# Optimization experiments

Hardware: AMD Instinct MI355X
Metric: run time of the kernel (lower is better)

Reference implementation:

```python
import jax, jax.numpy as jnp
import numpy as np

N = 50000
E = 800000
DIMS = [128, 128, 128, 64, 64]  # n_input, hidden[0], hidden[1], hidden[2], n_output


def setup_inputs() -> dict:
    key = jax.random.key(0)
    ks = jax.random.split(key, 16)
    x = jax.random.normal(ks[0], (N, DIMS[0]), dtype=jnp.float32)
    edge_index = jax.random.randint(ks[1], (2, E), 0, N, dtype=jnp.int64)
    inp = {"x": x, "edge_index": edge_index}
    for i in range(4):
        fan_in, fan_out = DIMS[i], DIMS[i + 1]
        scale = 1.0 / jnp.sqrt(jnp.float32(fan_in))
        inp[f"W{i+1}"] = jax.random.normal(ks[2 + 2 * i], (fan_in, fan_out), dtype=jnp.float32) * scale
        inp[f"b{i+1}"] = jnp.zeros((fan_out,), dtype=jnp.float32)
    return inp


def _gcn_norm(edge_index):
    # add self-loops, compute symmetric normalization D^-1/2 (A+I) D^-1/2
    loop = jnp.arange(N, dtype=edge_index.dtype)
    src = jnp.concatenate([edge_index[0], loop])
    dst = jnp.concatenate([edge_index[1], loop])
    ones = jnp.ones(src.shape[0], dtype=jnp.float32)
    deg = jax.ops.segment_sum(ones, dst, num_segments=N)
    dinv = jnp.where(deg > 0, jax.lax.rsqrt(deg), 0.0)
    norm = dinv[src] * dinv[dst]  # [E+N]
    return src, dst, norm


def _gcn_conv(x, W, b, src, dst, norm):
    h = x @ W                                   # [N, out]
    msg = h[src] * norm[:, None]                # gather + scale, [E+N, out]
    agg = jax.ops.segment_sum(msg, dst, num_segments=N)
    return agg + b


def reference(x, edge_index, W1, b1, W2, b2, W3, b3, W4, b4):
    src, dst, norm = _gcn_norm(edge_index)
    h = _gcn_conv(x, W1, b1, src, dst, norm)
    h = jax.nn.selu(h)
    h = _gcn_conv(h, W2, b2, src, dst, norm)
    h = jax.nn.selu(h)
    h = _gcn_conv(h, W3, b3, src, dst, norm)
    h = jax.nn.selu(h)
    h = _gcn_conv(h, W4, b4, src, dst, norm)
    # F.normalize(x): L2 row-normalize with eps=1e-12
    nrm = jnp.sqrt(jnp.sum(h * h, axis=1, keepdims=True))
    return h / jnp.maximum(nrm, 1e-12)
```

## Files before the change

kernel.cpp:

```cpp
#include <hip/hip_runtime.h>
#include <math.h>

#define NN 50000
#define NE 800000
#define NBK ((NN + 255) >> 8)
#define EPB 4096
#define BINA_BLOCKS ((NE + EPB - 1) / EPB)
#define EPT (EPB / 256)

typedef __attribute__((ext_vector_type(8))) __bf16 bf16x8;
typedef __attribute__((ext_vector_type(4))) float f32x4;

__device__ __forceinline__ float selu_f(float x) {
    const float scale = 1.0507009873554805f;
    const float alpha = 1.6732632423543772f;
    return scale * (x > 0.0f ? x : alpha * expm1f(x));
}

__device__ __forceinline__ unsigned rnd_bf16(float f) {
    unsigned u = __float_as_uint(f);
    return (u + 0x7fffu + ((u >> 16) & 1u)) >> 16;
}
__device__ __forceinline__ unsigned pack_pair(float a, float b) {
    return (rnd_bf16(b) << 16) | rnd_bf16(a);
}
__device__ __forceinline__ float lo_f(unsigned u) { return __uint_as_float(u << 16); }
__device__ __forceinline__ float hi_f(unsigned u) { return __uint_as_float(u & 0xffff0000u); }

__global__ void k_hist(const int* __restrict__ dst, int* __restrict__ cnt) {
    int e = blockIdx.x * blockDim.x + threadIdx.x;
    if (e < NE) atomicAdd(&cnt[dst[e]], 1);
}

#define NB1 ((NN + 1023) / 1024)

__global__ void k_scanA(const int* __restrict__ cnt, int* __restrict__ rowptr,
                        int* __restrict__ partials, float* __restrict__ dinv) {
    __shared__ int wsum[4];
    int tid = threadIdx.x;
    int lane = tid & 63, wave = tid >> 6;
    int base = blockIdx.x * 1024 + tid * 4;
    int e0 = 0, e1 = 0, e2 = 0, e3 = 0;
    if (base + 3 < NN) {
        int4 v = *(const int4*)&cnt[base];
        e0 = v.x; e1 = v.y; e2 = v.z; e3 = v.w;
    } else {
        if (base + 0 < NN) e0 = cnt[base + 0];
        if (base + 1 < NN) e1 = cnt[base + 1];
        if (base + 2 < NN) e2 = cnt[base + 2];
        if (base + 3 < NN) e3 = cnt[base + 3];
    }
    if (base + 0 < NN) dinv[base + 0] = rsqrtf((float)(e0 + 1));
    if (base + 1 < NN) dinv[base + 1] = rsqrtf((float)(e1 + 1));
    if (base + 2 < NN) dinv[base + 2] = rsqrtf((float)(e2 + 1));
    if (base + 3 < NN) dinv[base + 3] = rsqrtf((float)(e3 + 1));

    int lsum = e0 + e1 + e2 + e3;
    int s = lsum;
    #pragma unroll
    for (int off = 1; off < 64; off <<= 1) {
        int t = __shfl_up(s, off, 64);
        if (lane >= off) s += t;
    }
    if (lane == 63) wsum[wave] = s;
    __syncthreads();
    int wbase = 0;
    #pragma unroll
    for (int w = 0; w < 4; w++) wbase += (w < wave) ? wsum[w] : 0;
    int excl = wbase + s - lsum;
    if (base + 0 < NN) rowptr[base + 0] = excl;
    if (base + 1 < NN) rowptr[base + 1] = excl + e0;
    if (base + 2 < NN) rowptr[base + 2] = excl + e0 + e1;
    if (base + 3 < NN) rowptr[base + 3] = excl + e0 + e1 + e2;
    if (tid == 0)
        partials[blockIdx.x] = wsum[0] + wsum[1] + wsum[2] + wsum[3];
}

__global__ void k_scanB(int* __restrict__ partials, int* __restrict__ partials2,
                        int* __restrict__ rowptr) {
    int lane = threadIdx.x;
    int v = (lane < NB1) ? partials[lane] : 0;
    int s = v;
    #pragma unroll
    for (int off = 1; off < 64; off <<= 1) {
        int t = __shfl_up(s, off, 64);
        if (lane >= off) s += t;
    }
    if (lane < NB1) partials2[lane] = s - v;
    if (lane == 63) rowptr[NN] = s;
}

__global__ void k_scanC(int* __restrict__ rowptr, const int* __restrict__ partials2,
                        int* __restrict__ bcur) {
    int off = partials2[blockIdx.x];
    int base = blockIdx.x * 1024 + threadIdx.x * 4;
    #pragma unroll
    for (int j = 0; j < 4; j++) {
        int idx = base + j;
        if (idx < NN) {
            int r = rowptr[idx] + off;
            rowptr[idx] = r;
            if ((idx & 255) == 0) bcur[(idx >> 8) * 16] = r;
        }
    }
}

__global__ void __launch_bounds__(256) k_binA(const int* __restrict__ src,
                                              const int* __restrict__ dst,
                                              int* __restrict__ bcur,
                                              int* __restrict__ tmp) {
    __shared__ int hist[NBK];
    __shared__ int gbase[NBK];
    int tid = threadIdx.x;
    for (int i = tid; i < NBK; i += 256) hist[i] = 0;
    __syncthreads();

    const int e0 = blockIdx.x * EPB;
    int rec[EPT];
    int bs[EPT];
    #pragma unroll
    for (int j = 0; j < EPT; j++) {
        int e = e0 + j * 256 + tid;
        if (e < NE) {
            int s = src[e], d = dst[e];
            int b = d >> 8;
            int slot = atomicAdd(&hist[b], 1);
            rec[j] = (s << 8) | (d & 255);
            bs[j] = (b << 16) | slot;
        } else {
            bs[j] = -1;
        }
    }
    __syncthreads();
    for (int i = tid; i < NBK; i += 256)
        gbase[i] = atomicAdd(&bcur[i * 16], hist[i]);
    __syncthreads();
    #pragma unroll
    for (int j = 0; j < EPT; j++) {
        if (bs[j] >= 0) {
            int b = bs[j] >> 16, slot = bs[j] & 0xffff;
            tmp[gbase[b] + slot] = rec[j];
        }
    }
}

__global__ void __launch_bounds__(256) k_binB(const int* __restrict__ tmp,
                                              const int* __restrict__ rowptr,
                                              const float* __restrict__ dinv,
                                              int2* __restrict__ edat) {
    __shared__ int lpos[256];
    __shared__ float ldin[256];
    int b = blockIdx.x, tid = threadIdx.x;
    int n0 = b << 8;
    int n = n0 + tid;
    if (n < NN) { lpos[tid] = rowptr[n]; ldin[tid] = dinv[n]; }
    int base = rowptr[n0];
    int end  = rowptr[(n0 + 256 < NN) ? n0 + 256 : NN];
    __syncthreads();
    for (int i = base + tid; i < end; i += 256) {
        int rc = tmp[i];
        int s = rc >> 8;
        int dl = rc & 255;
        float nm = dinv[s] * ldin[dl];
        int slot = atomicAdd(&lpos[dl], 1);
        edat[slot] = make_int2(s, __float_as_int(nm));
    }
}

__global__ void k_packx(const float* __restrict__ x, unsigned* __restrict__ tabX) {
    long u = (long)blockIdx.x * 256 + threadIdx.x;
    if (u * 4 < (long)NN * 64) {
        const float4* ip = (const float4*)&x[u * 8];
        float4 a = ip[0], b = ip[1];
        uint4 o;
        o.x = pack_pair(a.x, a.y); o.y = pack_pair(a.z, a.w);
        o.z = pack_pair(b.x, b.y); o.w = pack_pair(b.z, b.w);
        *(uint4*)&tabX[u * 4] = o;
    }
}

__global__ void k_packw(const float* __restrict__ W1, const float* __restrict__ W2,
                        const float* __restrict__ W3, const float* __restrict__ W4,
                        unsigned* __restrict__ Wp) {
    int u = blockIdx.x * 256 + threadIdx.x;
    const float* W; int J, K2, off;
    if (u < 8192)       { W = W1; J = 128; K2 = 64; off = 0; }
    else if (u < 16384) { W = W2; J = 128; K2 = 64; off = 8192; }
    else if (u < 20480) { W = W3; J = 64;  K2 = 64; off = 16384; }
    else if (u < 22528) { W = W4; J = 64;  K2 = 32; off = 20480; }
    else return;
    int v = u - off;
    int col = v / K2, kk = v % K2;
    Wp[u] = pack_pair(W[(2 * kk) * J + col], W[(2 * kk + 1) * J + col]);
}

template <int K, int J>
__global__ void __launch_bounds__(256) k_mm4(const unsigned* __restrict__ tabin,
                                             const unsigned* __restrict__ Wp,
                                             unsigned* __restrict__ out) {
    constexpr int K2 = K / 2;
    constexpr int STRIDE = K2 + 4;
    constexpr int CT = J / 16;
    constexpr int KC = K / 32;
    constexpr int J2 = J / 2;

    __shared__ unsigned Wt[J * STRIDE];

    for (int u4 = threadIdx.x; u4 < J * K2 / 4; u4 += 256) {
        int v = u4 * 4;
        int col = v / K2, kk = v % K2;
        *(uint4*)&Wt[col * STRIDE + kk] = *(const uint4*)&Wp[v];
    }
    __syncthreads();

    const int w = threadIdx.x >> 6, l = threadIdx.x & 63;
    const int lr = l & 15, lk = l >> 4;
    const long r0 = (long)blockIdx.x * 128 + w * 32;

    f32x4 acc[CT][2];
    #pragma unroll
    for (int t = 0; t < CT; t++) {
        acc[t][0] = (f32x4)(0.0f);
        acc[t][1] = (f32x4)(0.0f);
    }

    #pragma unroll
    for (int kc = 0; kc < KC; kc++) {
        uint4 a0u = *(const uint4*)&tabin[(r0 + lr) * K2 + kc * 16 + lk * 4];
        uint4 a1u = *(const uint4*)&tabin[(r0 + 16 + lr) * K2 + kc * 16 + lk * 4];
        bf16x8 a0 = __builtin_bit_cast(bf16x8, a0u);
        bf16x8 a1 = __builtin_bit_cast(bf16x8, a1u);
        #pragma unroll
        for (int t = 0; t < CT; t++) {
            uint4 bu = *(const uint4*)&Wt[(t * 16 + lr) * STRIDE + kc * 16 + lk * 4];
            bf16x8 b = __builtin_bit_cast(bf16x8, bu);
            acc[t][0] = __builtin_amdgcn_mfma_f32_16x16x32_bf16(a0, b, acc[t][0], 0, 0, 0);
            acc[t][1] = __builtin_amdgcn_mfma_f32_16x16x32_bf16(a1, b, acc[t][1], 0, 0, 0);
        }
    }

    #pragma unroll
    for (int t = 0; t < CT; t++) {
        #pragma unroll
        for (int s = 0; s < 2; s++) {
            f32x4 d = acc[t][s];
            #pragma unroll
            for (int i = 0; i < 4; i++) {
                float v = d[i];
                float vp = __shfl_xor(v, 1);
                long row = r0 + s * 16 + lk * 4 + i;
                if (!(l & 1) && row < NN)
                    out[row * J2 + t * 8 + (lr >> 1)] = pack_pair(v, vp);
            }
        }
    }
}

template <bool DO_SELU>
__global__ void k_agg128w(const unsigned* __restrict__ tab, const int* __restrict__ rowptr,
                          const int2* __restrict__ edat, const float* __restrict__ dinv,
                          const float* __restrict__ bias, unsigned* __restrict__ outp) {
    int n = (blockIdx.x * blockDim.x + threadIdx.x) >> 6;
    int l = threadIdx.x & 63;
    if (n >= NN) return;
    int g = l >> 4, sub = l & 15;
    int beg = rowptr[n], end = rowptr[n + 1];

    float ax[8] = {0.f, 0.f, 0.f, 0.f, 0.f, 0.f, 0.f, 0.f};
    int e = beg + g;
    for (; e + 4 < end; e += 8) {
        int2 m0 = edat[e], m1 = edat[e + 4];
        uint4 v0 = *(const uint4*)&tab[(size_t)m0.x * 64 + sub * 4];
        uint4 v1 = *(const uint4*)&tab[(size_t)m1.x * 64 + sub * 4];
        float w0 = __int_as_float(m0.y), w1 = __int_as_float(m1.y);
        ax[0] += w0 * lo_f(v0.x); ax[1] += w0 * hi_f(v0.x);
        ax[2] += w0 * lo_f(v0.y); ax[3] += w0 * hi_f(v0.y);
        ax[4] += w0 * lo_f(v0.z); ax[5] += w0 * hi_f(v0.z);
        ax[6] += w0 * lo_f(v0.w); ax[7] += w0 * hi_f(v0.w);
        ax[0] += w1 * lo_f(v1.x); ax[1] += w1 * hi_f(v1.x);
        ax[2] += w1 * lo_f(v1.y); ax[3] += w1 * hi_f(v1.y);
        ax[4] += w1 * lo_f(v1.z); ax[5] += w1 * hi_f(v1.z);
        ax[6] += w1 * lo_f(v1.w); ax[7] += w1 * hi_f(v1.w);
    }
    for (; e < end; e += 4) {
        int2 m = edat[e];
        uint4 v = *(const uint4*)&tab[(size_t)m.x * 64 + sub * 4];
        float w = __int_as_float(m.y);
        ax[0] += w * lo_f(v.x); ax[1] += w * hi_f(v.x);
        ax[2] += w * lo_f(v.y); ax[3] += w * hi_f(v.y);
        ax[4] += w * lo_f(v.z); ax[5] += w * hi_f(v.z);
        ax[6] += w * lo_f(v.w); ax[7] += w * hi_f(v.w);
    }
    #pragma unroll
    for (int d = 0; d < 8; d++) {
        ax[d] += __shfl_xor(ax[d], 16);
        ax[d] += __shfl_xor(ax[d], 32);
    }
    if (g == 0) {
        float dn = dinv[n];
        float self = dn * dn;
        uint4 su = *(const uint4*)&tab[(size_t)n * 64 + sub * 4];
        float4 b0 = *(const float4*)&bias[sub * 8];
        float4 b1 = *(const float4*)&bias[sub * 8 + 4];
        ax[0] += b0.x + self * lo_f(su.x); ax[1] += b0.y + self * hi_f(su.x);
        ax[2] += b0.z + self * lo_f(su.y); ax[3] += b0.w + self * hi_f(su.y);
        ax[4] += b1.x + self * lo_f(su.z); ax[5] += b1.y + self * hi_f(su.z);
        ax[6] += b1.z + self * lo_f(su.w); ax[7] += b1.w + self * hi_f(su.w);
        if constexpr (DO_SELU) {
            #pragma unroll
            for (int d = 0; d < 8; d++) ax[d] = selu_f(ax[d]);
        }
        uint4 o;
        o.x = pack_pair(ax[0], ax[1]); o.y = pack_pair(ax[2], ax[3]);
        o.z = pack_pair(ax[4], ax[5]); o.w = pack_pair(ax[6], ax[7]);
        *(uint4*)&outp[(size_t)n * 64 + sub * 4] = o;
    }
}

template <bool DO_SELU, bool DO_NORM, bool PACK>
__global__ void k_agg64w(const unsigned* __restrict__ tab, const int* __restrict__ rowptr,
                         const int2* __restrict__ edat, const float* __restrict__ dinv,
                         const float* __restrict__ bias, void* __restrict__ out_) {
    int n = (blockIdx.x * blockDim.x + threadIdx.x) >> 6;
    int l = threadIdx.x & 63;
    if (n >= NN) return;
    int g = l >> 3, sub = l & 7;
    int beg = rowptr[n], end = rowptr[n + 1];

    float ax[8] = {0.f, 0.f, 0.f, 0.f, 0.f, 0.f, 0.f, 0.f};
    int e = beg + g;
    for (; e + 8 < end; e += 16) {
        int2 m0 = edat[e], m1 = edat[e + 8];
        uint4 v0 = *(const uint4*)&tab[(size_t)m0.x * 32 + sub * 4];
        uint4 v1 = *(const uint4*)&tab[(size_t)m1.x * 32 + sub * 4];
        float w0 = __int_as_float(m0.y), w1 = __int_as_float(m1.y);
        ax[0] += w0 * lo_f(v0.x); ax[1] += w0 * hi_f(v0.x);
        ax[2] += w0 * lo_f(v0.y); ax[3] += w0 * hi_f(v0.y);
        ax[4] += w0 * lo_f(v0.z); ax[5] += w0 * hi_f(v0.z);
        ax[6] += w0 * lo_f(v0.w); ax[7] += w0 * hi_f(v0.w);
        ax[0] += w1 * lo_f(v1.x); ax[1] += w1 * hi_f(v1.x);
        ax[2] += w1 * lo_f(v1.y); ax[3] += w1 * hi_f(v1.y);
        ax[4] += w1 * lo_f(v1.z); ax[5] += w1 * hi_f(v1.z);
        ax[6] += w1 * lo_f(v1.w); ax[7] += w1 * hi_f(v1.w);
    }
    for (; e < end; e += 8) {
        int2 m = edat[e];
        uint4 v = *(const uint4*)&tab[(size_t)m.x * 32 + sub * 4];
        float w = __int_as_float(m.y);
        ax[0] += w * lo_f(v.x); ax[1] += w * hi_f(v.x);
        ax[2] += w * lo_f(v.y); ax[3] += w * hi_f(v.y);
        ax[4] += w * lo_f(v.z); ax[5] += w * hi_f(v.z);
        ax[6] += w * lo_f(v.w); ax[7] += w * hi_f(v.w);
    }
    #pragma unroll
    for (int d = 0; d < 8; d++) {
        ax[d] += __shfl_xor(ax[d], 8);
        ax[d] += __shfl_xor(ax[d], 16);
        ax[d] += __shfl_xor(ax[d], 32);
    }
    if (g == 0) {
        float dn = dinv[n];
        float self = dn * dn;
        uint4 su = *(const uint4*)&tab[(size_t)n * 32 + sub * 4];
        float4 b0 = *(const float4*)&bias[sub * 8];
        float4 b1 = *(const float4*)&bias[sub * 8 + 4];
        ax[0] += b0.x + self * lo_f(su.x); ax[1] += b0.y + self * hi_f(su.x);
        ax[2] += b0.z + self * lo_f(su.y); ax[3] += b0.w + self * hi_f(su.y);
        ax[4] += b1.x + self * lo_f(su.z); ax[5] += b1.y + self * hi_f(su.z);
        ax[6] += b1.z + self * lo_f(su.w); ax[7] += b1.w + self * hi_f(su.w);
        if constexpr (DO_SELU) {
            #pragma unroll
            for (int d = 0; d < 8; d++) ax[d] = selu_f(ax[d]);
        }
        if constexpr (DO_NORM) {
            float ss = 0.f;
            #pragma unroll
            for (int d = 0; d < 8; d++) ss += ax[d] * ax[d];
            ss += __shfl_xor(ss, 1);
            ss += __shfl_xor(ss, 2);
            ss += __shfl_xor(ss, 4);
            float inv = 1.0f / fmaxf(sqrtf(ss), 1e-12f);
            #pragma unroll
            for (int d = 0; d < 8; d++) ax[d] *= inv;
        }
        if constexpr (PACK) {
            uint4 o;
            o.x = pack_pair(ax[0], ax[1]); o.y = pack_pair(ax[2], ax[3]);
            o.z = pack_pair(ax[4], ax[5]); o.w = pack_pair(ax[6], ax[7]);
            *(uint4*)&((unsigned*)out_)[(size_t)n * 32 + sub * 4] = o;
        } else {
            float* op = (float*)out_ + (size_t)n * 64 + sub * 8;
            *(float4*)op = make_float4(ax[0], ax[1], ax[2], ax[3]);
            *(float4*)(op + 4) = make_float4(ax[4], ax[5], ax[6], ax[7]);
        }
    }
}

extern "C" void kernel_launch(void* const* d_in, const int* in_sizes, int n_in,
                              void* d_out, int out_size, void* d_ws, size_t ws_size,
                              hipStream_t stream) {
    const float* x  = (const float*)d_in[0];
    const int* edge = (const int*)d_in[1];
    const float* W1 = (const float*)d_in[2]; const float* b1 = (const float*)d_in[3];
    const float* W2 = (const float*)d_in[4]; const float* b2 = (const float*)d_in[5];
    const float* W3 = (const float*)d_in[6]; const float* b3 = (const float*)d_in[7];
    const float* W4 = (const float*)d_in[8]; const float* b4 = (const float*)d_in[9];
    float* out = (float*)d_out;

    char* ws = (char*)d_ws;
    size_t off = 0;
    auto alloc = [&](size_t bytes) -> void* {
        void* p = ws + off;
        off = (off + bytes + 255) & ~(size_t)255;
        return p;
    };
    int*      cnt    = (int*)alloc((size_t)NN * 4);
    int*      rowptr = (int*)alloc((size_t)(NN + 1) * 4);
    float*    dinv   = (float*)alloc((size_t)NN * 4);
    int*      tmp    = (int*)alloc((size_t)NE * 4);
    int2*     edat   = (int2*)alloc((size_t)NE * 8);
    unsigned* tabX   = (unsigned*)alloc((size_t)(NN + 128) * 64 * 4);
    unsigned* tab    = (unsigned*)alloc((size_t)(NN + 128) * 64 * 4);
    unsigned* bufU   = (unsigned*)alloc((size_t)(NN + 128) * 64 * 4);
    unsigned* Wp     = (unsigned*)alloc((size_t)22528 * 4);
    int*      part1  = (int*)alloc(64 * 4);
    int*      part2  = (int*)alloc(64 * 4);
    int*      bcur   = (int*)alloc((size_t)NBK * 16 * 4);

    const int* srcp = edge;
    const int* dstp = edge + NE;

    const int BE = (NE + 255) / 256;

    hipMemsetAsync(cnt, 0, (size_t)NN * 4, stream);
    k_hist<<<BE, 256, 0, stream>>>(dstp, cnt);
    k_scanA<<<NB1, 256, 0, stream>>>(cnt, rowptr, part1, dinv);
    k_scanB<<<1, 64, 0, stream>>>(part1, part2, rowptr);
    k_scanC<<<NB1, 256, 0, stream>>>(rowptr, part2, bcur);
    k_binA<<<BINA_BLOCKS, 256, 0, stream>>>(srcp, dstp, bcur, tmp);
    k_binB<<<NBK, 256, 0, stream>>>(tmp, rowptr, dinv, edat);

    const int AGG_B = (NN + 3) / 4;
    const int MMB = (NN + 127) / 128;
    const int PXB = ((NN * 64 / 4) + 255) / 256;

    k_packw<<<88, 256, 0, stream>>>(W1, W2, W3, W4, Wp);
    k_packx<<<PXB, 256, 0, stream>>>(x, tabX);

    k_mm4<128, 128><<<MMB, 256, 0, stream>>>(tabX, Wp, tab);
    k_agg128w<true><<<AGG_B, 256, 0, stream>>>(tab, rowptr, edat, dinv, b1, bufU);
    k_mm4<128, 128><<<MMB, 256, 0, stream>>>(bufU, Wp + 8192, tab);
    k_agg128w<true><<<AGG_B, 256, 0, stream>>>(tab, rowptr, edat, dinv, b2, bufU);
    k_mm4<128, 64><<<MMB, 256, 0, stream>>>(bufU, Wp + 16384, tab);
    k_agg64w<true, false, true><<<AGG_B, 256, 0, stream>>>(tab, rowptr, edat, dinv, b3, bufU);
    k_mm4<64, 64><<<MMB, 256, 0, stream>>>(bufU, Wp + 20480, tab);
    k_agg64w<false, true, false><<<AGG_B, 256, 0, stream>>>(tab, rowptr, edat, dinv, b4, out);
}
```

Measured before the change: 336.8 us.

## Fold source-side normalization into GEMM epilogue and build CSR with bucket-level scan

Pre-scales each GEMM output row by dinv[row], so aggregation sums plain neighbor rows and applies dinv[dst] once at the end. This lets the per-edge record shrink from an (index, weight) pair to a column index only, halving edge metadata traffic and removing a multiply per edge. The CSR build replaces the per-node histogram and three-stage scan with a bucket histogram and a single-block scan; per-node counts, rowptr and dinv are computed inside the second binning pass. The x-to-bf16 packing kernel is fused into the first GEMM's load path. Rounding changes slightly because the scale is applied before the bf16 conversion.

```diff
diff --git a/kernel.cpp b/kernel.cpp
--- a/kernel.cpp
+++ b/kernel.cpp
@@ -27,36 +27,29 @@
 __device__ __forceinline__ float lo_f(unsigned u) { return __uint_as_float(u << 16); }
 __device__ __forceinline__ float hi_f(unsigned u) { return __uint_as_float(u & 0xffff0000u); }
 
-__global__ void k_hist(const int* __restrict__ dst, int* __restrict__ cnt) {
-    int e = blockIdx.x * blockDim.x + threadIdx.x;
-    if (e < NE) atomicAdd(&cnt[dst[e]], 1);
-}
-
-#define NB1 ((NN + 1023) / 1024)
-
-__global__ void k_scanA(const int* __restrict__ cnt, int* __restrict__ rowptr,
-                        int* __restrict__ partials, float* __restrict__ dinv) {
+__global__ void __launch_bounds__(256) k_histB(const int* __restrict__ dst,
+                                               int* __restrict__ bhist) {
+    __shared__ int h[NBK];
+    for (int i = threadIdx.x; i < NBK; i += 256) h[i] = 0;
+    __syncthreads();
+    int e0 = blockIdx.x * EPB;
+    #pragma unroll
+    for (int j = 0; j < EPT; j++) {
+        int e = e0 + j * 256 + threadIdx.x;
+        if (e < NE) atomicAdd(&h[dst[e] >> 8], 1);
+    }
+    __syncthreads();
+    for (int i = threadIdx.x; i < NBK; i += 256)
+        if (h[i]) atomicAdd(&bhist[i], h[i]);
+}
+
+__global__ void k_scanBkt(const int* __restrict__ bhist, int* __restrict__ bbase,
+                          int* __restrict__ bcur, int* __restrict__ rowptr) {
     __shared__ int wsum[4];
     int tid = threadIdx.x;
     int lane = tid & 63, wave = tid >> 6;
-    int base = blockIdx.x * 1024 + tid * 4;
-    int e0 = 0, e1 = 0, e2 = 0, e3 = 0;
-    if (base + 3 < NN) {
-        int4 v = *(const int4*)&cnt[base];
-        e0 = v.x; e1 = v.y; e2 = v.z; e3 = v.w;
-    } else {
-        if (base + 0 < NN) e0 = cnt[base + 0];
-        if (base + 1 < NN) e1 = cnt[base + 1];
-        if (base + 2 < NN) e2 = cnt[base + 2];
-        if (base + 3 < NN) e3 = cnt[base + 3];
-    }
-    if (base + 0 < NN) dinv[base + 0] = rsqrtf((float)(e0 + 1));
-    if (base + 1 < NN) dinv[base + 1] = rsqrtf((float)(e1 + 1));
-    if (base + 2 < NN) dinv[base + 2] = rsqrtf((float)(e2 + 1));
-    if (base + 3 < NN) dinv[base + 3] = rsqrtf((float)(e3 + 1));
-
-    int lsum = e0 + e1 + e2 + e3;
-    int s = lsum;
+    int v = (tid < NBK) ? bhist[tid] : 0;
+    int s = v;
     #pragma unroll
     for (int off = 1; off < 64; off <<= 1) {
         int t = __shfl_up(s, off, 64);
@@ -67,42 +60,9 @@
     int wbase = 0;
     #pragma unroll
     for (int w = 0; w < 4; w++) wbase += (w < wave) ? wsum[w] : 0;
-    int excl = wbase + s - lsum;
-    if (base + 0 < NN) rowptr[base + 0] = excl;
-    if (base + 1 < NN) rowptr[base + 1] = excl + e0;
-    if (base + 2 < NN) rowptr[base + 2] = excl + e0 + e1;
-    if (base + 3 < NN) rowptr[base + 3] = excl + e0 + e1 + e2;
-    if (tid == 0)
-        partials[blockIdx.x] = wsum[0] + wsum[1] + wsum[2] + wsum[3];
-}
-
-__global__ void k_scanB(int* __restrict__ partials, int* __restrict__ partials2,
-                        int* __restrict__ rowptr) {
-    int lane = threadIdx.x;
-    int v = (lane < NB1) ? partials[lane] : 0;
-    int s = v;
-    #pragma unroll
-    for (int off = 1; off < 64; off <<= 1) {
-        int t = __shfl_up(s, off, 64);
-        if (lane >= off) s += t;
-    }
-    if (lane < NB1) partials2[lane] = s - v;
-    if (lane == 63) rowptr[NN] = s;
-}
-
-__global__ void k_scanC(int* __restrict__ rowptr, const int* __restrict__ partials2,
-                        int* __restrict__ bcur) {
-    int off = partials2[blockIdx.x];
-    int base = blockIdx.x * 1024 + threadIdx.x * 4;
-    #pragma unroll
-    for (int j = 0; j < 4; j++) {
-        int idx = base + j;
-        if (idx < NN) {
-            int r = rowptr[idx] + off;
-            rowptr[idx] = r;
-            if ((idx & 255) == 0) bcur[(idx >> 8) * 16] = r;
-        }
-    }
+    int excl = wbase + s - v;
+    if (tid < NBK) { bbase[tid] = excl; bcur[tid * 16] = excl; }
+    if (tid == 0) { bbase[NBK] = NE; rowptr[NN] = NE; }
 }
 
 __global__ void __launch_bounds__(256) k_binA(const int* __restrict__ src,
@@ -144,38 +104,47 @@
     }
 }
 
-__global__ void __launch_bounds__(256) k_binB(const int* __restrict__ tmp,
-                                              const int* __restrict__ rowptr,
-                                              const float* __restrict__ dinv,
-                                              int2* __restrict__ edat) {
+__global__ void __launch_bounds__(256) k_cntB(const int* __restrict__ tmp,
+                                              const int* __restrict__ bbase,
+                                              int* __restrict__ rowptr,
+                                              float* __restrict__ dinv,
+                                              int* __restrict__ ecol) {
+    __shared__ int cnt256[256];
     __shared__ int lpos[256];
-    __shared__ float ldin[256];
+    __shared__ int wsum[4];
     int b = blockIdx.x, tid = threadIdx.x;
     int n0 = b << 8;
+    cnt256[tid] = 0;
+    __syncthreads();
+    int base = bbase[b], end = bbase[b + 1];
+    for (int i = base + tid; i < end; i += 256)
+        atomicAdd(&cnt256[tmp[i] & 255], 1);
+    __syncthreads();
+    int c = cnt256[tid];
+    int lane = tid & 63, wave = tid >> 6;
+    int s = c;
+    #pragma unroll
+    for (int off = 1; off < 64; off <<= 1) {
+        int t = __shfl_up(s, off, 64);
+        if (lane >= off) s += t;
+    }
+    if (lane == 63) wsum[wave] = s;
+    __syncthreads();
+    int wbase = 0;
+    #pragma unroll
+    for (int w = 0; w < 4; w++) wbase += (w < wave) ? wsum[w] : 0;
+    int excl = base + wbase + s - c;
     int n = n0 + tid;
-    if (n < NN) { lpos[tid] = rowptr[n]; ldin[tid] = dinv[n]; }
-    int base = rowptr[n0];
-    int end  = rowptr[(n0 + 256 < NN) ? n0 + 256 : NN];
+    if (n < NN) {
+        rowptr[n] = excl;
+        dinv[n] = rsqrtf((float)(c + 1));
+    }
+    lpos[tid] = excl;
     __syncthreads();
     for (int i = base + tid; i < end; i += 256) {
         int rc = tmp[i];
-        int s = rc >> 8;
-        int dl = rc & 255;
-        float nm = dinv[s] * ldin[dl];
-        int slot = atomicAdd(&lpos[dl], 1);
-        edat[slot] = make_int2(s, __float_as_int(nm));
-    }
-}
-
-__global__ void k_packx(const float* __restrict__ x, unsigned* __restrict__ tabX) {
-    long u = (long)blockIdx.x * 256 + threadIdx.x;
-    if (u * 4 < (long)NN * 64) {
-        const float4* ip = (const float4*)&x[u * 8];
-        float4 a = ip[0], b = ip[1];
-        uint4 o;
-        o.x = pack_pair(a.x, a.y); o.y = pack_pair(a.z, a.w);
-        o.z = pack_pair(b.x, b.y); o.w = pack_pair(b.z, b.w);
-        *(uint4*)&tabX[u * 4] = o;
+        int slot = atomicAdd(&lpos[rc & 255], 1);
+        ecol[slot] = rc >> 8;
     }
 }
 
@@ -194,9 +163,10 @@
     Wp[u] = pack_pair(W[(2 * kk) * J + col], W[(2 * kk + 1) * J + col]);
 }
 
-template <int K, int J>
-__global__ void __launch_bounds__(256) k_mm4(const unsigned* __restrict__ tabin,
+template <int K, int J, bool INF32>
+__global__ void __launch_bounds__(256) k_mm4(const void* __restrict__ in_,
                                              const unsigned* __restrict__ Wp,
+                                             const float* __restrict__ dinv,
                                              unsigned* __restrict__ out) {
     constexpr int K2 = K / 2;
     constexpr int STRIDE = K2 + 4;
@@ -226,8 +196,24 @@
 
     #pragma unroll
     for (int kc = 0; kc < KC; kc++) {
-        uint4 a0u = *(const uint4*)&tabin[(r0 + lr) * K2 + kc * 16 + lk * 4];
-        uint4 a1u = *(const uint4*)&tabin[(r0 + 16 + lr) * K2 + kc * 16 + lk * 4];
+        uint4 a0u, a1u;
+        if constexpr (INF32) {
+            const float* xin = (const float*)in_;
+            long ra0 = r0 + lr;      if (ra0 >= NN) ra0 = NN - 1;
+            long ra1 = r0 + 16 + lr; if (ra1 >= NN) ra1 = NN - 1;
+            const float4* p0 = (const float4*)&xin[ra0 * K + kc * 32 + lk * 8];
+            const float4* p1 = (const float4*)&xin[ra1 * K + kc * 32 + lk * 8];
+            float4 fa = p0[0], fb = p0[1];
+            a0u.x = pack_pair(fa.x, fa.y); a0u.y = pack_pair(fa.z, fa.w);
+            a0u.z = pack_pair(fb.x, fb.y); a0u.w = pack_pair(fb.z, fb.w);
+            float4 ga = p1[0], gb = p1[1];
+            a1u.x = pack_pair(ga.x, ga.y); a1u.y = pack_pair(ga.z, ga.w);
+            a1u.z = pack_pair(gb.x, gb.y); a1u.w = pack_pair(gb.z, gb.w);
+        } else {
+            const unsigned* tabin = (const unsigned*)in_;
+            a0u = *(const uint4*)&tabin[(r0 + lr) * K2 + kc * 16 + lk * 4];
+            a1u = *(const uint4*)&tabin[(r0 + 16 + lr) * K2 + kc * 16 + lk * 4];
+        }
         bf16x8 a0 = __builtin_bit_cast(bf16x8, a0u);
         bf16x8 a1 = __builtin_bit_cast(bf16x8, a1u);
         #pragma unroll
@@ -249,8 +235,10 @@
                 float v = d[i];
                 float vp = __shfl_xor(v, 1);
                 long row = r0 + s * 16 + lk * 4 + i;
-                if (!(l & 1) && row < NN)
-                    out[row * J2 + t * 8 + (lr >> 1)] = pack_pair(v, vp);
+                if (!(l & 1) && row < NN) {
+                    float sc = dinv[row];
+                    out[row * J2 + t * 8 + (lr >> 1)] = pack_pair(v * sc, vp * sc);
+                }
             }
         }
     }
@@ -258,7 +246,7 @@
 
 template <bool DO_SELU>
 __global__ void k_agg128w(const unsigned* __restrict__ tab, const int* __restrict__ rowptr,
-                          const int2* __restrict__ edat, const float* __restrict__ dinv,
+                          const int* __restrict__ ecol, const float* __restrict__ dinv,
                           const float* __restrict__ bias, unsigned* __restrict__ outp) {
     int n = (blockIdx.x * blockDim.x + threadIdx.x) >> 6;
     int l = threadIdx.x & 63;
@@ -269,27 +257,25 @@
     float ax[8] = {0.f, 0.f, 0.f, 0.f, 0.f, 0.f, 0.f, 0.f};
     int e = beg + g;
     for (; e + 4 < end; e += 8) {
-        int2 m0 = edat[e], m1 = edat[e + 4];
-        uint4 v0 = *(const uint4*)&tab[(size_t)m0.x * 64 + sub * 4];
-        uint4 v1 = *(const uint4*)&tab[(size_t)m1.x * 64 + sub * 4];
-        float w0 = __int_as_float(m0.y), w1 = __int_as_float(m1.y);
-        ax[0] += w0 * lo_f(v0.x); ax[1] += w0 * hi_f(v0.x);
-        ax[2] += w0 * lo_f(v0.y); ax[3] += w0 * hi_f(v0.y);
-        ax[4] += w0 * lo_f(v0.z); ax[5] += w0 * hi_f(v0.z);
-        ax[6] += w0 * lo_f(v0.w); ax[7] += w0 * hi_f(v0.w);
-        ax[0] += w1 * lo_f(v1.x); ax[1] += w1 * hi_f(v1.x);
-        ax[2] += w1 * lo_f(v1.y); ax[3] += w1 * hi_f(v1.y);
-        ax[4] += w1 * lo_f(v1.z); ax[5] += w1 * hi_f(v1.z);
-        ax[6] += w1 * lo_f(v1.w); ax[7] += w1 * hi_f(v1.w);
+        int s0 = ecol[e], s1 = ecol[e + 4];
+        uint4 v0 = *(const uint4*)&tab[(size_t)s0 * 64 + sub * 4];
+        uint4 v1 = *(const uint4*)&tab[(size_t)s1 * 64 + sub * 4];
+        ax[0] += lo_f(v0.x); ax[1] += hi_f(v0.x);
+        ax[2] += lo_f(v0.y); ax[3] += hi_f(v0.y);
+        ax[4] += lo_f(v0.z); ax[5] += hi_f(v0.z);
+        ax[6] += lo_f(v0.w); ax[7] += hi_f(v0.w);
+        ax[0] += lo_f(v1.x); ax[1] += hi_f(v1.x);
+        ax[2] += lo_f(v1.y); ax[3] += hi_f(v1.y);
+        ax[4] += lo_f(v1.z); ax[5] += hi_f(v1.z);
+        ax[6] += lo_f(v1.w); ax[7] += hi_f(v1.w);
     }
     for (; e < end; e += 4) {
-        int2 m = edat[e];
-        uint4 v = *(const uint4*)&tab[(size_t)m.x * 64 + sub * 4];
-        float w = __int_as_float(m.y);
-        ax[0] += w * lo_f(v.x); ax[1] += w * hi_f(v.x);
-        ax[2] += w * lo_f(v.y); ax[3] += w * hi_f(v.y);
-        ax[4] += w * lo_f(v.z); ax[5] += w * hi_f(v.z);
-        ax[6] += w * lo_f(v.w); ax[7] += w * hi_f(v.w);
+        int s0 = ecol[e];
+        uint4 v = *(const uint4*)&tab[(size_t)s0 * 64 + sub * 4];
+        ax[0] += lo_f(v.x); ax[1] += hi_f(v.x);
+        ax[2] += lo_f(v.y); ax[3] += hi_f(v.y);
+        ax[4] += lo_f(v.z); ax[5] += hi_f(v.z);
+        ax[6] += lo_f(v.w); ax[7] += hi_f(v.w);
     }
     #pragma unroll
     for (int d = 0; d < 8; d++) {
@@ -298,14 +284,17 @@
     }
     if (g == 0) {
         float dn = dinv[n];
-        float self = dn * dn;
         uint4 su = *(const uint4*)&tab[(size_t)n * 64 + sub * 4];
+        ax[0] += lo_f(su.x); ax[1] += hi_f(su.x);
+        ax[2] += lo_f(su.y); ax[3] += hi_f(su.y);
+        ax[4] += lo_f(su.z); ax[5] += hi_f(su.z);
+        ax[6] += lo_f(su.w); ax[7] += hi_f(su.w);
         float4 b0 = *(const float4*)&bias[sub * 8];
         float4 b1 = *(const float4*)&bias[sub * 8 + 4];
-        ax[0] += b0.x + self * lo_f(su.x); ax[1] += b0.y + self * hi_f(su.x);
-        ax[2] += b0.z + self * lo_f(su.y); ax[3] += b0.w + self * hi_f(su.y);
-        ax[4] += b1.x + self * lo_f(su.z); ax[5] += b1.y + self * hi_f(su.z);
-        ax[6] += b1.z + self * lo_f(su.w); ax[7] += b1.w + self * hi_f(su.w);
+        ax[0] = b0.x + dn * ax[0]; ax[1] = b0.y + dn * ax[1];
+        ax[2] = b0.z + dn * ax[2]; ax[3] = b0.w + dn * ax[3];
+        ax[4] = b1.x + dn * ax[4]; ax[5] = b1.y + dn * ax[5];
+        ax[6] = b1.z + dn * ax[6]; ax[7] = b1.w + dn * ax[7];
         if constexpr (DO_SELU) {
             #pragma unroll
             for (int d = 0; d < 8; d++) ax[d] = selu_f(ax[d]);
@@ -319,7 +308,7 @@
 
 template <bool DO_SELU, bool DO_NORM, bool PACK>
 __global__ void k_agg64w(const unsigned* __restrict__ tab, const int* __restrict__ rowptr,
-                         const int2* __restrict__ edat, const float* __restrict__ dinv,
+                         const int* __restrict__ ecol, const float* __restrict__ dinv,
                          const float* __restrict__ bias, void* __restrict__ out_) {
     int n = (blockIdx.x * blockDim.x + threadIdx.x) >> 6;
     int l = threadIdx.x & 63;
@@ -330,27 +319,25 @@
     float ax[8] = {0.f, 0.f, 0.f, 0.f, 0.f, 0.f, 0.f, 0.f};
     int e = beg + g;
     for (; e + 8 < end; e += 16) {
-        int2 m0 = edat[e], m1 = edat[e + 8];
-        uint4 v0 = *(const uint4*)&tab[(size_t)m0.x * 32 + sub * 4];
-        uint4 v1 = *(const uint4*)&tab[(size_t)m1.x * 32 + sub * 4];
-        float w0 = __int_as_float(m0.y), w1 = __int_as_float(m1.y);
-        ax[0] += w0 * lo_f(v0.x); ax[1] += w0 * hi_f(v0.x);
-        ax[2] += w0 * lo_f(v0.y); ax[3] += w0 * hi_f(v0.y);
-        ax[4] += w0 * lo_f(v0.z); ax[5] += w0 * hi_f(v0.z);
-        ax[6] += w0 * lo_f(v0.w); ax[7] += w0 * hi_f(v0.w);
-        ax[0] += w1 * lo_f(v1.x); ax[1] += w1 * hi_f(v1.x);
-        ax[2] += w1 * lo_f(v1.y); ax[3] += w1 * hi_f(v1.y);
-        ax[4] += w1 * lo_f(v1.z); ax[5] += w1 * hi_f(v1.z);
-        ax[6] += w1 * lo_f(v1.w); ax[7] += w1 * hi_f(v1.w);
+        int s0 = ecol[e], s1 = ecol[e + 8];
+        uint4 v0 = *(const uint4*)&tab[(size_t)s0 * 32 + sub * 4];
+        uint4 v1 = *(const uint4*)&tab[(size_t)s1 * 32 + sub * 4];
+        ax[0] += lo_f(v0.x); ax[1] += hi_f(v0.x);
+        ax[2] += lo_f(v0.y); ax[3] += hi_f(v0.y);
+        ax[4] += lo_f(v0.z); ax[5] += hi_f(v0.z);
+        ax[6] += lo_f(v0.w); ax[7] += hi_f(v0.w);
+        ax[0] += lo_f(v1.x); ax[1] += hi_f(v1.x);
+        ax[2] += lo_f(v1.y); ax[3] += hi_f(v1.y);
+        ax[4] += lo_f(v1.z); ax[5] += hi_f(v1.z);
+        ax[6] += lo_f(v1.w); ax[7] += hi_f(v1.w);
     }
     for (; e < end; e += 8) {
-        int2 m = edat[e];
-        uint4 v = *(const uint4*)&tab[(size_t)m.x * 32 + sub * 4];
-        float w = __int_as_float(m.y);
-        ax[0] += w * lo_f(v.x); ax[1] += w * hi_f(v.x);
-        ax[2] += w * lo_f(v.y); ax[3] += w * hi_f(v.y);
-        ax[4] += w * lo_f(v.z); ax[5] += w * hi_f(v.z);
-        ax[6] += w * lo_f(v.w); ax[7] += w * hi_f(v.w);
+        int s0 = ecol[e];
+        uint4 v = *(const uint4*)&tab[(size_t)s0 * 32 + sub * 4];
+        ax[0] += lo_f(v.x); ax[1] += hi_f(v.x);
+        ax[2] += lo_f(v.y); ax[3] += hi_f(v.y);
+        ax[4] += lo_f(v.z); ax[5] += hi_f(v.z);
+        ax[6] += lo_f(v.w); ax[7] += hi_f(v.w);
     }
     #pragma unroll
     for (int d = 0; d < 8; d++) {
@@ -360,14 +347,17 @@
     }
     if (g == 0) {
         float dn = dinv[n];
-        float self = dn * dn;
         uint4 su = *(const uint4*)&tab[(size_t)n * 32 + sub * 4];
+        ax[0] += lo_f(su.x); ax[1] += hi_f(su.x);
+        ax[2] += lo_f(su.y); ax[3] += hi_f(su.y);
+        ax[4] += lo_f(su.z); ax[5] += hi_f(su.z);
+        ax[6] += lo_f(su.w); ax[7] += hi_f(su.w);
         float4 b0 = *(const float4*)&bias[sub * 8];
         float4 b1 = *(const float4*)&bias[sub * 8 + 4];
-        ax[0] += b0.x + self * lo_f(su.x); ax[1] += b0.y + self * hi_f(su.x);
-        ax[2] += b0.z + self * lo_f(su.y); ax[3] += b0.w + self * hi_f(su.y);
-        ax[4] += b1.x + self * lo_f(su.z); ax[5] += b1.y + self * hi_f(su.z);
-        ax[6] += b1.z + self * lo_f(su.w); ax[7] += b1.w + self * hi_f(su.w);
+        ax[0] = b0.x + dn * ax[0]; ax[1] = b0.y + dn * ax[1];
+        ax[2] = b0.z + dn * ax[2]; ax[3] = b0.w + dn * ax[3];
+        ax[4] = b1.x + dn * ax[4]; ax[5] = b1.y + dn * ax[5];
+        ax[6] = b1.z + dn * ax[6]; ax[7] = b1.w + dn * ax[7];
         if constexpr (DO_SELU) {
             #pragma unroll
             for (int d = 0; d < 8; d++) ax[d] = selu_f(ax[d]);
@@ -414,45 +404,37 @@
         off = (off + bytes + 255) & ~(size_t)255;
         return p;
     };
-    int*      cnt    = (int*)alloc((size_t)NN * 4);
     int*      rowptr = (int*)alloc((size_t)(NN + 1) * 4);
     float*    dinv   = (float*)alloc((size_t)NN * 4);
     int*      tmp    = (int*)alloc((size_t)NE * 4);
-    int2*     edat   = (int2*)alloc((size_t)NE * 8);
-    unsigned* tabX   = (unsigned*)alloc((size_t)(NN + 128) * 64 * 4);
+    int*      ecol   = (int*)alloc((size_t)NE * 4);
     unsigned* tab    = (unsigned*)alloc((size_t)(NN + 128) * 64 * 4);
     unsigned* bufU   = (unsigned*)alloc((size_t)(NN + 128) * 64 * 4);
     unsigned* Wp     = (unsigned*)alloc((size_t)22528 * 4);
-    int*      part1  = (int*)alloc(64 * 4);
-    int*      part2  = (int*)alloc(64 * 4);
+    int*      bhist  = (int*)alloc((size_t)NBK * 4);
+    int*      bbase  = (int*)alloc((size_t)(NBK + 1) * 4);
     int*      bcur   = (int*)alloc((size_t)NBK * 16 * 4);
 
     const int* srcp = edge;
     const int* dstp = edge + NE;
 
-    const int BE = (NE + 255) / 256;
-
-    hipMemsetAsync(cnt, 0, (size_t)NN * 4, stream);
-    k_hist<<<BE, 256, 0, stream>>>(dstp, cnt);
-    k_scanA<<<NB1, 256, 0, stream>>>(cnt, rowptr, part1, dinv);
-    k_scanB<<<1, 64, 0, stream>>>(part1, part2, rowptr);
-    k_scanC<<<NB1, 256, 0, stream>>>(rowptr, part2, bcur);
+    hipMemsetAsync(bhist, 0, (size_t)NBK * 4, stream);
+    k_histB<<<BINA_BLOCKS, 256, 0, stream>>>(dstp, bhist);
+    k_scanBkt<<<1, 256, 0, stream>>>(bhist, bbase, bcur, rowptr);
     k_binA<<<BINA_BLOCKS, 256, 0, stream>>>(srcp, dstp, bcur, tmp);
-    k_binB<<<NBK, 256, 0, stream>>>(tmp, rowptr, dinv, edat);
+    k_cntB<<<NBK, 256, 0, stream>>>(tmp, bbase, rowptr, dinv, ecol);
 
     const int AGG_B = (NN + 3) / 4;
     const int MMB = (NN + 127) / 128;
-    const int PXB = ((NN * 64 / 4) + 255) / 256;
 
     k_packw<<<88, 256, 0, stream>>>(W1, W2, W3, W4, Wp);
-    k_packx<<<PXB, 256, 0, stream>>>(x, tabX);
-
-    k_mm4<128, 128><<<MMB, 256, 0, stream>>>(tabX, Wp, tab);
-    k_agg128w<true><<<AGG_B, 256, 0, stream>>>(tab, rowptr, edat, dinv, b1, bufU);
-    k_mm4<128, 128><<<MMB, 256, 0, stream>>>(bufU, Wp + 8192, tab);
-    k_agg128w<true><<<AGG_B, 256, 0, stream>>>(tab, rowptr, edat, dinv, b2, bufU);
-    k_mm4<128, 64><<<MMB, 256, 0, stream>>>(bufU, Wp + 16384, tab);
-    k_agg64w<true, false, true><<<AGG_B, 256, 0, stream>>>(tab, rowptr, edat, dinv, b3, bufU);
-    k_mm4<64, 64><<<MMB, 256, 0, stream>>>(bufU, Wp + 20480, tab);
-    k_agg64w<false, true, false><<<AGG_B, 256, 0, stream>>>(tab, rowptr, edat, dinv, b4, out);
-}
+
+    k_mm4<128, 128, true><<<MMB, 256, 0, stream>>>(x, Wp, dinv, tab);
+    k_agg128w<true><<<AGG_B, 256, 0, stream>>>(tab, rowptr, ecol, dinv, b1, bufU);
+    k_mm4<128, 128, false><<<MMB, 256, 0, stream>>>(bufU, Wp + 8192, dinv, tab);
+    k_agg128w<true><<<AGG_B, 256, 0, stream>>>(tab, rowptr, ecol, dinv, b2, bufU);
+    k_mm4<128, 64, false><<<MMB, 256, 0, stream>>>(bufU, Wp + 16384, dinv, tab);
+    k_agg64w<true, false, true><<<AGG_B, 256, 0, stream>>>(tab, rowptr, ecol, dinv, b3, bufU);
+    k_mm4<64, 64, false><<<MMB, 256, 0, stream>>>(bufU, Wp + 20480, dinv, tab);
+    k_agg64w<false, true, false><<<AGG_B, 256, 0, stream>>>(tab, rowptr, ecol, dinv, b4, out);
+}
```

Result: faster. 320.2 us (-4.9%).
